# Kernel tuning notes

Hardware: AMD Instinct MI355X
Metric: run time of the kernel (lower is better)

The kernel has to match this reference:

```python
import jax, jax.numpy as jnp
import numpy as np
from jax import lax

VOCAB = 50000
EMB = 300
HID = 256
N = 4096          # total_sents
T_COL = 64
T_ROW = 16
N_DOCS = 512


def setup_inputs() -> dict:
    key = jax.random.key(0)
    ks = jax.random.split(key, 20)

    def glorot(k, shape):
        fan = float(sum(shape))
        return (jax.random.normal(k, shape, jnp.float32) * (2.0 / fan) ** 0.5)

    inp = {}
    inp["col"] = jax.random.randint(ks[0], (N, T_COL), 0, VOCAB, dtype=jnp.int32)
    inp["row"] = jax.random.randint(ks[1], (N, T_ROW), 0, VOCAB, dtype=jnp.int32)
    inp["row_neg"] = jax.random.randint(ks[2], (N, T_ROW), 0, VOCAB, dtype=jnp.int32)
    # pack_padded_sequence expects lengths sorted descending
    inp["col_lens"] = jnp.sort(jax.random.randint(ks[3], (N,), 1, T_COL + 1, dtype=jnp.int32))[::-1]
    inp["row_lens"] = jnp.sort(jax.random.randint(ks[4], (N,), 1, T_ROW + 1, dtype=jnp.int32))[::-1]
    inp["row_neg_lens"] = jnp.sort(jax.random.randint(ks[5], (N,), 1, T_ROW + 1, dtype=jnp.int32))[::-1]
    inp["col_refs"] = jax.random.randint(ks[6], (N,), 0, N_DOCS, dtype=jnp.int32)
    inp["row_refs"] = jax.random.randint(ks[7], (N,), 0, N_DOCS, dtype=jnp.int32)
    inp["row_neg_refs"] = jax.random.randint(ks[8], (N,), 0, N_DOCS, dtype=jnp.int32)
    inp["embed_table"] = jax.random.normal(ks[9], (VOCAB, EMB), jnp.float32) * 0.1
    inp["col_W_ih"] = glorot(ks[10], (4 * HID, EMB))
    inp["col_W_hh"] = glorot(ks[11], (4 * HID, HID))
    inp["col_b_ih"] = jnp.zeros((4 * HID,), jnp.float32)
    inp["col_b_hh"] = jnp.zeros((4 * HID,), jnp.float32)
    inp["row_W_ih"] = glorot(ks[12], (4 * HID, EMB))
    inp["row_W_hh"] = glorot(ks[13], (4 * HID, HID))
    inp["row_b_ih"] = jnp.zeros((4 * HID,), jnp.float32)
    inp["row_b_hh"] = jnp.zeros((4 * HID,), jnp.float32)
    return inp


def lstm_last_hidden(x, lengths, W_ih, W_hh, b_ih, b_hh):
    """x: [N,T,E]; returns hidden state at step lengths-1 per sequence: [N,H].
    Equivalent to torch LSTM over a packed padded sequence (state frozen past len)."""
    Nn, T, _ = x.shape
    H = W_hh.shape[1]
    h0 = jnp.zeros((Nn, H), x.dtype)
    bias = b_ih + b_hh

    def step(carry, inputs):
        h, c = carry
        xt, t = inputs  # xt: [N,E]
        gates = xt @ W_ih.T + h @ W_hh.T + bias  # [N,4H]
        i, f, g, o = jnp.split(gates, 4, axis=-1)  # torch gate order i,f,g,o
        i = jax.nn.sigmoid(i); f = jax.nn.sigmoid(f); o = jax.nn.sigmoid(o)
        g = jnp.tanh(g)
        c_new = f * c + i * g
        h_new = o * jnp.tanh(c_new)
        m = (t < lengths)[:, None]
        return (jnp.where(m, h_new, h), jnp.where(m, c_new, c)), None

    (h, _), _ = lax.scan(step, (h0, h0), (jnp.swapaxes(x, 0, 1), jnp.arange(T)))
    return h


def reference(col, row, row_neg, col_lens, row_lens, row_neg_lens,
              col_refs, row_refs, row_neg_refs, embed_table,
              col_W_ih, col_W_hh, col_b_ih, col_b_hh,
              row_W_ih, row_W_hh, row_b_ih, row_b_hh):
    # Dropout is identity (eval-mode reference).
    def compose(tokens, lens, refs, W_ih, W_hh, b_ih, b_hh):
        emb = embed_table[tokens]                      # [N,T,E]
        h = lstm_last_hidden(emb, lens, W_ih, W_hh, b_ih, b_hh)  # [N,H]
        # mask-multiply + sum == segment-sum of hidden states by doc ref,
        # scattered into a [total_sents, H] buffer (rows >= n_docs are zero)
        return jax.ops.segment_sum(h, refs, num_segments=tokens.shape[0])

    col_h = compose(col, col_lens, col_refs, col_W_ih, col_W_hh, col_b_ih, col_b_hh)
    row_h = compose(row, row_lens, row_refs, row_W_ih, row_W_hh, row_b_ih, row_b_hh)
    neg_h = compose(row_neg, row_neg_lens, row_neg_refs, row_W_ih, row_W_hh, row_b_ih, row_b_hh)

    pos = jnp.sum(col_h * row_h, axis=1)
    neg = jnp.sum(col_h * neg_h, axis=1)
    # BPRLoss(size_average=False): sum of -logsigmoid(pos - neg)
    return -jnp.sum(jax.nn.log_sigmoid(pos - neg))
```

## Files before the change

### kernel.cpp

```cpp
#include <hip/hip_runtime.h>


typedef __bf16 bf16x8 __attribute__((ext_vector_type(8)));
typedef float  fvec4  __attribute__((ext_vector_type(4)));

#define NSEN 4096
#define HIDN 256
#define EMBD 300
#define VOC  50000

#define OFF_P     0ULL
#define OFF_BPK   204800000ULL
#define OFF_WHHC  206110720ULL
#define OFF_WHHR  206635008ULL
#define OFF_BIAS  207159296ULL
#define OFF_SEG   219750400ULL
#define OFF_LOSS  232333312ULL

static __device__ __forceinline__ unsigned short f2bf(float x) {
    unsigned int u = __float_as_uint(x);
    unsigned int r = (u + 0x7fffu + ((u >> 16) & 1u)) >> 16;
    return (unsigned short)r;
}
static __device__ __forceinline__ float bf2f(unsigned short b) {
    return __uint_as_float(((unsigned int)b) << 16);
}
static __device__ __forceinline__ float sigm(float x) { return 1.f / (1.f + __expf(-x)); }
static __device__ __forceinline__ float tanh_(float x) {
    float e = __expf(2.f * x);
    return 1.f - 2.f / (e + 1.f);
}
static __device__ __forceinline__ fvec4 unpk(uint2 v) {
    fvec4 o;
    o[0] = __uint_as_float((v.x & 0xffffu) << 16);
    o[1] = __uint_as_float(v.x & 0xffff0000u);
    o[2] = __uint_as_float((v.y & 0xffffu) << 16);
    o[3] = __uint_as_float(v.y & 0xffff0000u);
    return o;
}

static __device__ __forceinline__ void gld_lds16(const unsigned short* g,
                                                 unsigned short* l)
{
    __builtin_amdgcn_global_load_lds(
        (const __attribute__((address_space(1))) unsigned int*)g,
        (__attribute__((address_space(3))) unsigned int*)l, 16, 0, 0);
}

static __device__ __forceinline__ int whh_src(int o) {
    int L  = o >> 9;
    int r9 = o & 511;
    int ln = r9 >> 3, j = r9 & 7;
    int g  = L & 3, kt = (L >> 2) & 7, wv = (L >> 5) & 15;
    int row = g * 256 + wv * 16 + (ln & 15);
    int col = kt * 32 + (ln >> 4) * 8 + j;
    return row * 256 + col;
}

__global__ void prep_kernel(
    const float* __restrict__ cWih, const float* __restrict__ rWih,
    const float* __restrict__ cWhh, const float* __restrict__ rWhh,
    const float* __restrict__ cbih, const float* __restrict__ cbhh,
    const float* __restrict__ rbih, const float* __restrict__ rbhh,
    unsigned short* __restrict__ Bpk, unsigned short* __restrict__ WhhC,
    unsigned short* __restrict__ WhhR, float* __restrict__ biascat)
{
    int idx = blockIdx.x * 256 + threadIdx.x;
    if (idx < 655360) {
        int e = idx & 511, lnn = e >> 3, j = e & 7;
        int f = idx >> 9;
        int ntt = f & 3;
        int kc = f >> 2;
        int kt = kc % 10;
        int s  = kc / 10;
        int n = (s >> 1) * 128 + (s & 1) * 64 + ntt * 16 + (lnn & 15);
        int k = kt * 32 + (lnn >> 4) * 8 + j;
        float v = 0.f;
        if (k < EMBD) v = (n < 1024) ? cWih[n * EMBD + k] : rWih[(n - 1024) * EMBD + k];
        Bpk[idx] = f2bf(v);
        return;
    }
    idx -= 655360;
    if (idx < 262144) { WhhC[idx] = f2bf(cWhh[whh_src(idx)]); return; }
    idx -= 262144;
    if (idx < 262144) { WhhR[idx] = f2bf(rWhh[whh_src(idx)]); return; }
    idx -= 262144;
    if (idx < 2048)
        biascat[idx] = (idx < 1024) ? (cbih[idx] + cbhh[idx])
                                    : (rbih[idx - 1024] + rbhh[idx - 1024]);
}

__global__ __launch_bounds__(256) void gemm_p_kernel(
    const float* __restrict__ A,
    const unsigned short* __restrict__ Bpk,
    const float* __restrict__ bias,
    unsigned short* __restrict__ Pout)
{
    const int mb = blockIdx.x * 128;
    const int tid = threadIdx.x;
    const int wv = tid >> 6, ln = tid & 63, l15 = ln & 15, q = ln >> 4;
    const int wm = wv & 1, wn = wv >> 1;

    __shared__ __align__(16) unsigned short At[2][4][10][512];

    {
        int row = tid >> 1, kh = tid & 1;
        int gr = mb + row;
        unsigned short* dst = &At[row >> 6][(row >> 4) & 3][0][0];
        const int fl = row & 15;
        #pragma unroll
        for (int i = 0; i < 40; ++i) {
            int k = kh * 160 + i * 4;
            float4 v = make_float4(0.f, 0.f, 0.f, 0.f);
            if (gr < VOC && k < EMBD)
                v = *(const float4*)(A + (size_t)gr * EMBD + k);
            ushort4 b;
            b.x = f2bf(v.x); b.y = f2bf(v.y); b.z = f2bf(v.z); b.w = f2bf(v.w);
            int di = (k >> 5) * 512 + ((k >> 3) & 3) * 128 + fl * 8 + (k & 7);
            *(ushort4*)(dst + di) = b;
        }
    }
    __syncthreads();

    for (int nc = 0; nc < 16; ++nc) {
        fvec4 acc[4][4];
        #pragma unroll
        for (int a = 0; a < 4; ++a)
            #pragma unroll
            for (int b = 0; b < 4; ++b) acc[a][b] = (fvec4)0.f;

        #pragma unroll 2
        for (int kt = 0; kt < 10; ++kt) {
            const unsigned short* bp =
                Bpk + (size_t)(((nc * 2 + wn) * 10 + kt) * 4) * 512 + ln * 8;
            bf16x8 bfr[4];
            #pragma unroll
            for (int ntt = 0; ntt < 4; ++ntt)
                bfr[ntt] = *(const bf16x8*)(bp + ntt * 512);
            #pragma unroll
            for (int mt = 0; mt < 4; ++mt) {
                bf16x8 af = *(const bf16x8*)&At[wm][mt][kt][ln * 8];
                #pragma unroll
                for (int ntt = 0; ntt < 4; ++ntt)
                    acc[mt][ntt] = __builtin_amdgcn_mfma_f32_16x16x32_bf16(
                        af, bfr[ntt], acc[mt][ntt], 0, 0, 0);
            }
        }
        float bv[4];
        #pragma unroll
        for (int ntt = 0; ntt < 4; ++ntt)
            bv[ntt] = bias[nc * 128 + wn * 64 + ntt * 16 + l15];
        #pragma unroll
        for (int mt = 0; mt < 4; ++mt) {
            #pragma unroll
            for (int r = 0; r < 4; ++r) {
                int m = mb + wm * 64 + mt * 16 + q * 4 + r;
                if (m < VOC) {
                    size_t base = (size_t)m * 2048 + nc * 128 + wn * 64;
                    #pragma unroll
                    for (int ntt = 0; ntt < 4; ++ntt)
                        Pout[base + ntt * 16 + l15] = f2bf(acc[mt][ntt][r] + bv[ntt]);
                }
            }
        }
    }
}

__global__ __launch_bounds__(1024, 2) void lstm_kernel(
    const int* __restrict__ colTok, const int* __restrict__ rowTok, const int* __restrict__ negTok,
    const int* __restrict__ colLen, const int* __restrict__ rowLen, const int* __restrict__ negLen,
    const int* __restrict__ crefs, const int* __restrict__ rrefs, const int* __restrict__ nrefs,
    const unsigned short* __restrict__ P,
    const unsigned short* __restrict__ WhhC, const unsigned short* __restrict__ WhhR,
    float* __restrict__ seg)
{
    const int part = blockIdx.x >> 8;
    const int sb = blockIdx.x & 255;
    const int s0 = sb * 16;
    const int* tok = part == 0 ? colTok : (part == 1 ? rowTok : negTok);
    const int* len = part == 0 ? colLen : (part == 1 ? rowLen : negLen);
    const int* refs = part == 0 ? crefs : (part == 1 ? rrefs : nrefs);
    const unsigned short* Whh = part == 0 ? WhhC : WhhR;
    const int T = part == 0 ? 64 : 16;
    const int pco = part == 0 ? 0 : 1024;
    float* segp = seg + (size_t)part * 1048576;

    const int tid = threadIdx.x;
    const int wv = tid >> 6;
    const int ln = tid & 63, l15 = ln & 15, q = ln >> 4;

    __shared__ __align__(16) unsigned short hx[2][8][4][16][8];
    __shared__ __align__(16) unsigned short pstage[16][4][2][16][8];
    char* hB0 = (char*)&hx[0][0][0][0][0];
    char* hB1 = (char*)&hx[1][0][0][0][0];

    for (int i = tid; i < 8192; i += 1024) (&hx[0][0][0][0][0])[i] = 0;

    const int len0 = len[s0 + l15];
    int ml = len0;
    #pragma unroll
    for (int off = 1; off < 16; off <<= 1) ml = max(ml, __shfl_xor(ml, off));
    const int maxlen = ml;

    const unsigned short* wbase = Whh + (size_t)wv * 16384 + (size_t)ln * 8;

    const int wrByte = (wv >> 1) * 1024 + ((wv & 1) * 2 + (q >> 1)) * 256 +
                       l15 * 16 + (q & 1) * 8;

    const int dg = ln >> 5, dh = (ln >> 4) & 1;

    float c[4];
    #pragma unroll
    for (int r = 0; r < 4; ++r) c[r] = 0.f;
    ushort4 hpk = make_ushort4(0, 0, 0, 0);

    bf16x8 wres[4][4];
    #pragma unroll
    for (int kt = 0; kt < 4; ++kt)
        #pragma unroll
        for (int g = 0; g < 4; ++g)
            wres[kt][g] = *(const bf16x8*)(wbase + (size_t)(kt * 4 + g) * 512);

    __syncthreads();

    {
        int tk = tok[(s0 + l15) * T];
        #pragma unroll
        for (int d = 0; d < 2; ++d) {
            const unsigned short* src = P + (size_t)tk * 2048 + pco +
                (2 * d + dg) * 256 + wv * 16 + dh * 8;
            gld_lds16(src, &pstage[wv][2 * d][0][0][0]);
        }
    }
    int tknext = tok[(s0 + l15) * T + 1];

    for (int t = 0; t < maxlen; ++t) {
        const char* hRd = (t & 1) ? hB1 : hB0;
        char* hWr = (t & 1) ? hB0 : hB1;

        fvec4 acc[4];
        #pragma unroll
        for (int g = 0; g < 4; ++g) acc[g] = (fvec4)0.f;

        #pragma unroll
        for (int kt = 0; kt < 4; ++kt) {
            bf16x8 b0 = *(const bf16x8*)(hRd + kt * 1024 + ln * 16);
            #pragma unroll
            for (int g = 0; g < 4; ++g)
                acc[g] = __builtin_amdgcn_mfma_f32_16x16x32_bf16(
                    wres[kt][g], b0, acc[g], 0, 0, 0);
        }
        #pragma unroll 2
        for (int kt = 4; kt < 8; ++kt) {
            bf16x8 b0 = *(const bf16x8*)(hRd + kt * 1024 + ln * 16);
            #pragma unroll
            for (int g = 0; g < 4; ++g) {
                bf16x8 a = *(const bf16x8*)(wbase + (size_t)(kt * 4 + g) * 512);
                acc[g] = __builtin_amdgcn_mfma_f32_16x16x32_bf16(a, b0, acc[g], 0, 0, 0);
            }
        }

        asm volatile("s_waitcnt vmcnt(0)" ::: "memory");
        #pragma unroll
        for (int g = 0; g < 4; ++g) {
            fvec4 pv = unpk(*(const uint2*)
                &pstage[wv][g][q >> 1][l15][(q & 1) * 4]);
            acc[g] += pv;
        }

        if (t + 1 < maxlen) {
            asm volatile("s_waitcnt lgkmcnt(0)" ::: "memory");
            __builtin_amdgcn_sched_barrier(0);
            #pragma unroll
            for (int d = 0; d < 2; ++d) {
                const unsigned short* src = P + (size_t)tknext * 2048 + pco +
                    (2 * d + dg) * 256 + wv * 16 + dh * 8;
                gld_lds16(src, &pstage[wv][2 * d][0][0][0]);
            }
            int t2 = (t + 2 < T) ? (t + 2) : (T - 1);
            tknext = tok[(s0 + l15) * T + t2];
        }

        {
            bool act = t < len0;
            if (act) {
                float hr[4];
                #pragma unroll
                for (int r = 0; r < 4; ++r) {
                    float iv = acc[0][r];
                    float fv = acc[1][r];
                    float gv = acc[2][r];
                    float ov = acc[3][r];
                    float cn = sigm(fv) * c[r] + sigm(iv) * tanh_(gv);
                    c[r] = cn;
                    hr[r] = sigm(ov) * tanh_(cn);
                }
                hpk = make_ushort4(f2bf(hr[0]), f2bf(hr[1]),
                                   f2bf(hr[2]), f2bf(hr[3]));
            }
            *(ushort4*)(hWr + wrByte) = hpk;
        }
        asm volatile("s_waitcnt lgkmcnt(0)\n\ts_barrier" ::: "memory");
    }

    const char* hF = (maxlen & 1) ? hB1 : hB0;
    for (int i = tid; i < 16 * HIDN; i += 1024) {
        int sq = i >> 8, hd = i & 255;
        unsigned short hv = *(const unsigned short*)
            (hF + (hd >> 5) * 1024 + ((hd >> 3) & 3) * 256 +
             sq * 16 + (hd & 7) * 2);
        int rf = refs[s0 + sq];
        atomicAdd(segp + (size_t)rf * 256 + hd, bf2f(hv));
    }
}

__global__ void loss_kernel(const float* __restrict__ seg, float* __restrict__ part)
{
    int d = blockIdx.x, tid = threadIdx.x;
    const float* sc = seg + (size_t)d * 256;
    const float* sr = seg + 1048576 + (size_t)d * 256;
    const float* sn = seg + 2097152 + (size_t)d * 256;
    float a = sc[tid];
    float p = a * sr[tid];
    float n = a * sn[tid];
    for (int off = 32; off; off >>= 1) { p += __shfl_down(p, off); n += __shfl_down(n, off); }
    __shared__ float rp[4], rn[4];
    if ((tid & 63) == 0) { rp[tid >> 6] = p; rn[tid >> 6] = n; }
    __syncthreads();
    if (tid == 0) {
        float Ps = rp[0] + rp[1] + rp[2] + rp[3];
        float Ns = rn[0] + rn[1] + rn[2] + rn[3];
        float x = Ps - Ns;
        part[d] = fmaxf(-x, 0.f) + log1pf(expf(-fabsf(x)));
    }
}

__global__ void reduce_kernel(const float* __restrict__ part, float* __restrict__ out)
{
    int tid = threadIdx.x;
    float s = 0.f;
    for (int i = tid; i < 4096; i += 256) s += part[i];
    for (int off = 32; off; off >>= 1) s += __shfl_down(s, off);
    __shared__ float r[4];
    if ((tid & 63) == 0) r[tid >> 6] = s;
    __syncthreads();
    if (tid == 0) out[0] = r[0] + r[1] + r[2] + r[3];
}

extern "C" void kernel_launch(void* const* d_in, const int* in_sizes, int n_in,
                              void* d_out, int out_size, void* d_ws, size_t ws_size,
                              hipStream_t stream)
{
    const int*   col      = (const int*)d_in[0];
    const int*   row      = (const int*)d_in[1];
    const int*   rneg     = (const int*)d_in[2];
    const int*   col_lens = (const int*)d_in[3];
    const int*   row_lens = (const int*)d_in[4];
    const int*   rng_lens = (const int*)d_in[5];
    const int*   col_refs = (const int*)d_in[6];
    const int*   row_refs = (const int*)d_in[7];
    const int*   rng_refs = (const int*)d_in[8];
    const float* embed    = (const float*)d_in[9];
    const float* cWih     = (const float*)d_in[10];
    const float* cWhh     = (const float*)d_in[11];
    const float* cbih     = (const float*)d_in[12];
    const float* cbhh     = (const float*)d_in[13];
    const float* rWih     = (const float*)d_in[14];
    const float* rWhh     = (const float*)d_in[15];
    const float* rbih     = (const float*)d_in[16];
    const float* rbhh     = (const float*)d_in[17];

    char* ws = (char*)d_ws;
    unsigned short* P    = (unsigned short*)(ws + OFF_P);
    unsigned short* Bpk  = (unsigned short*)(ws + OFF_BPK);
    unsigned short* WhhC = (unsigned short*)(ws + OFF_WHHC);
    unsigned short* WhhR = (unsigned short*)(ws + OFF_WHHR);
    float* biascat = (float*)(ws + OFF_BIAS);
    float* seg     = (float*)(ws + OFF_SEG);
    float* lpart   = (float*)(ws + OFF_LOSS);

    hipMemsetAsync(seg, 0, 3 * 4096 * 256 * sizeof(float), stream);

    prep_kernel<<<4616, 256, 0, stream>>>(cWih, rWih, cWhh, rWhh,
                                          cbih, cbhh, rbih, rbhh,
                                          Bpk, WhhC, WhhR, biascat);
    gemm_p_kernel<<<391, 256, 0, stream>>>(embed, Bpk, biascat, P);
    lstm_kernel<<<768, 1024, 0, stream>>>(col, row, rneg,
                                          col_lens, row_lens, rng_lens,
                                          col_refs, row_refs, rng_refs,
                                          P, WhhC, WhhR, seg);
    loss_kernel<<<4096, 256, 0, stream>>>(seg, lpart);
    reduce_kernel<<<1, 256, 0, stream>>>(lpart, (float*)d_out);
}
```

Baseline: 601.4 us.

## Halve GEMM M-tile and stage output through LDS for coalesced stores

The embedding-projection GEMM now uses 64-row tiles, launching twice as many blocks. Each of the four waves covers 32 output columns, and the packed weight layout is reordered to match. Results are written into a padded LDS tile, then copied to global memory as 8-byte chunks instead of scattered 2-byte stores. This targets low occupancy and uncoalesced output writes to the large P buffer, at the cost of an extra LDS round trip, two syncs per column chunk, and less reuse of weights per block.

```diff
diff --git a/kernel.cpp b/kernel.cpp
--- a/kernel.cpp
+++ b/kernel.cpp
@@ -69,11 +69,11 @@
     if (idx < 655360) {
         int e = idx & 511, lnn = e >> 3, j = e & 7;
         int f = idx >> 9;
-        int ntt = f & 3;
-        int kc = f >> 2;
+        int ntt = f & 1;
+        int kc = f >> 1;
         int kt = kc % 10;
         int s  = kc / 10;
-        int n = (s >> 1) * 128 + (s & 1) * 64 + ntt * 16 + (lnn & 15);
+        int n = s * 32 + ntt * 16 + (lnn & 15);
         int k = kt * 32 + (lnn >> 4) * 8 + j;
         float v = 0.f;
         if (k < EMBD) v = (n < 1024) ? cWih[n * EMBD + k] : rWih[(n - 1024) * EMBD + k];
@@ -96,21 +96,22 @@
     const float* __restrict__ bias,
     unsigned short* __restrict__ Pout)
 {
-    const int mb = blockIdx.x * 128;
+    const int mb = blockIdx.x * 64;
     const int tid = threadIdx.x;
     const int wv = tid >> 6, ln = tid & 63, l15 = ln & 15, q = ln >> 4;
-    const int wm = wv & 1, wn = wv >> 1;
-
-    __shared__ __align__(16) unsigned short At[2][4][10][512];
+
+    __shared__ __align__(16) unsigned short At[4][10][512];
+    __shared__ __align__(16) unsigned short tile[64 * 132];
+    char* tileB = (char*)&tile[0];
 
     {
-        int row = tid >> 1, kh = tid & 1;
+        int row = tid >> 2, kh = tid & 3;
         int gr = mb + row;
-        unsigned short* dst = &At[row >> 6][(row >> 4) & 3][0][0];
         const int fl = row & 15;
-        #pragma unroll
-        for (int i = 0; i < 40; ++i) {
-            int k = kh * 160 + i * 4;
+        unsigned short* dst = &At[row >> 4][0][0];
+        #pragma unroll
+        for (int i = 0; i < 20; ++i) {
+            int k = kh * 80 + i * 4;
             float4 v = make_float4(0.f, 0.f, 0.f, 0.f);
             if (gr < VOC && k < EMBD)
                 v = *(const float4*)(A + (size_t)gr * EMBD + k);
@@ -123,45 +124,49 @@
     __syncthreads();
 
     for (int nc = 0; nc < 16; ++nc) {
-        fvec4 acc[4][4];
+        fvec4 acc[4][2];
         #pragma unroll
         for (int a = 0; a < 4; ++a)
             #pragma unroll
-            for (int b = 0; b < 4; ++b) acc[a][b] = (fvec4)0.f;
+            for (int b = 0; b < 2; ++b) acc[a][b] = (fvec4)0.f;
 
         #pragma unroll 2
         for (int kt = 0; kt < 10; ++kt) {
             const unsigned short* bp =
-                Bpk + (size_t)(((nc * 2 + wn) * 10 + kt) * 4) * 512 + ln * 8;
-            bf16x8 bfr[4];
-            #pragma unroll
-            for (int ntt = 0; ntt < 4; ++ntt)
-                bfr[ntt] = *(const bf16x8*)(bp + ntt * 512);
+                Bpk + (size_t)((((nc * 4 + wv) * 10 + kt) * 2)) * 512 + ln * 8;
+            bf16x8 bfr[2];
+            bfr[0] = *(const bf16x8*)(bp);
+            bfr[1] = *(const bf16x8*)(bp + 512);
             #pragma unroll
             for (int mt = 0; mt < 4; ++mt) {
-                bf16x8 af = *(const bf16x8*)&At[wm][mt][kt][ln * 8];
+                bf16x8 af = *(const bf16x8*)&At[mt][kt][ln * 8];
+                acc[mt][0] = __builtin_amdgcn_mfma_f32_16x16x32_bf16(af, bfr[0], acc[mt][0], 0, 0, 0);
+                acc[mt][1] = __builtin_amdgcn_mfma_f32_16x16x32_bf16(af, bfr[1], acc[mt][1], 0, 0, 0);
+            }
+        }
+
+        __syncthreads();
+        #pragma unroll
+        for (int mt = 0; mt < 4; ++mt)
+            #pragma unroll
+            for (int ntt = 0; ntt < 2; ++ntt) {
+                float bv = bias[nc * 128 + wv * 32 + ntt * 16 + l15];
                 #pragma unroll
-                for (int ntt = 0; ntt < 4; ++ntt)
-                    acc[mt][ntt] = __builtin_amdgcn_mfma_f32_16x16x32_bf16(
-                        af, bfr[ntt], acc[mt][ntt], 0, 0, 0);
-            }
-        }
-        float bv[4];
-        #pragma unroll
-        for (int ntt = 0; ntt < 4; ++ntt)
-            bv[ntt] = bias[nc * 128 + wn * 64 + ntt * 16 + l15];
-        #pragma unroll
-        for (int mt = 0; mt < 4; ++mt) {
-            #pragma unroll
-            for (int r = 0; r < 4; ++r) {
-                int m = mb + wm * 64 + mt * 16 + q * 4 + r;
-                if (m < VOC) {
-                    size_t base = (size_t)m * 2048 + nc * 128 + wn * 64;
-                    #pragma unroll
-                    for (int ntt = 0; ntt < 4; ++ntt)
-                        Pout[base + ntt * 16 + l15] = f2bf(acc[mt][ntt][r] + bv[ntt]);
-                }
-            }
+                for (int r = 0; r < 4; ++r)
+                    *(unsigned short*)(tileB + (mt * 16 + q * 4 + r) * 264 +
+                                       (wv * 32 + ntt * 16 + l15) * 2)
+                        = f2bf(acc[mt][ntt][r] + bv);
+            }
+        __syncthreads();
+
+        #pragma unroll
+        for (int it = 0; it < 8; ++it) {
+            int i = tid + it * 256;
+            int row = i >> 5, ch = i & 31;
+            uint2 v = *(const uint2*)(tileB + row * 264 + ch * 8);
+            int m = mb + row;
+            if (m < VOC)
+                *(uint2*)(Pout + (size_t)m * 2048 + nc * 128 + ch * 4) = v;
         }
     }
 }
@@ -384,7 +389,7 @@
     prep_kernel<<<4616, 256, 0, stream>>>(cWih, rWih, cWhh, rWhh,
                                           cbih, cbhh, rbih, rbhh,
                                           Bpk, WhhC, WhhR, biascat);
-    gemm_p_kernel<<<391, 256, 0, stream>>>(embed, Bpk, biascat, P);
+    gemm_p_kernel<<<782, 256, 0, stream>>>(embed, Bpk, biascat, P);
     lstm_kernel<<<768, 1024, 0, stream>>>(col, row, rneg,
                                           col_lens, row_lens, rng_lens,
                                           col_refs, row_refs, rng_refs,
```

Result: slower. 630.2 us (+4.8%).
